# Optimization experiments

Measured on AMD Instinct MI355X. Metric: run time of the kernel, lower is better.

## Reference

```python
import jax, jax.numpy as jnp
import numpy as np

B, T, V, S = 64, 512, 1296, 32
BLANK = 0
NEG = jnp.float32(-1e30)  # log-space -inf surrogate (keeps grads finite)


def setup_inputs() -> dict:
    key = jax.random.key(0)
    k1, k2 = jax.random.split(key)
    logits = jax.random.normal(k1, (B, T, V), dtype=jnp.float32)
    # CTC targets must not contain the blank index (0)
    targets = jax.random.randint(k2, (B, S), 1, V).astype(jnp.int64)
    input_lengths = jnp.full((B,), T, dtype=jnp.int32)
    target_lengths = jnp.full((B,), S, dtype=jnp.int32)
    return {"logits": logits, "targets": targets,
            "input_lengths": input_lengths, "target_lengths": target_lengths}


def _ctc_loss(log_probs, targets, input_lengths, target_lengths):
    """CTC negative log-likelihood, reduction='mean' (per-sample / target_len, then batch mean)."""
    Bb, Tt, Vv = log_probs.shape
    Ss = targets.shape[1]
    L = 2 * Ss + 1  # extended label sequence: blank-interleaved

    ext = jnp.full((Bb, L), BLANK, dtype=targets.dtype).at[:, 1::2].set(targets)  # (B,L)
    # log-prob of each extended label at each time: (B,T,L)
    lp_ext = jnp.take_along_axis(log_probs, jnp.broadcast_to(ext[:, None, :], (Bb, Tt, L)), axis=2)

    # transition s-2 -> s allowed iff ext[s] is non-blank (s odd) and ext[s] != ext[s-2]
    pos = jnp.arange(L)
    ext_m2 = jnp.pad(ext, ((0, 0), (2, 0)), constant_values=-1)[:, :L]
    skip_ok = (pos[None, :] % 2 == 1) & (ext != ext_m2)  # (B,L)

    alpha0 = (jnp.full((Bb, L), NEG)
              .at[:, 0].set(lp_ext[:, 0, 0])
              .at[:, 1].set(lp_ext[:, 0, 1]))

    def step(alpha, lp_t):
        a1 = alpha
        a2 = jnp.pad(alpha[:, :-1], ((0, 0), (1, 0)), constant_values=NEG)
        a3 = jnp.where(skip_ok, jnp.pad(alpha[:, :-2], ((0, 0), (2, 0)), constant_values=NEG), NEG)
        new = jnp.logaddexp(jnp.logaddexp(a1, a2), a3) + lp_t
        return new, new

    _, alphas_rest = jax.lax.scan(step, alpha0, jnp.swapaxes(lp_ext, 0, 1)[1:])  # (T-1,B,L)
    alphas = jnp.concatenate([alpha0[None], alphas_rest], axis=0)  # (T,B,L)

    bi = jnp.arange(Bb)
    alpha_last = alphas[input_lengths - 1, bi]  # (B,L)
    l_end = alpha_last[bi, 2 * target_lengths]       # final blank
    l_lab = alpha_last[bi, 2 * target_lengths - 1]   # final label
    nll = -jnp.logaddexp(l_end, l_lab)               # (B,)
    nll = jnp.where(jnp.isinf(nll) | (nll > 1e29), 0.0, nll)  # zero_infinity=True
    return jnp.mean(nll / target_lengths.astype(nll.dtype))    # reduction='mean'


def reference(logits, targets, input_lengths, target_lengths):
    log_probs = jax.nn.log_softmax(logits, axis=-1)
    return _ctc_loss(log_probs, targets, input_lengths, target_lengths)
```

## Files before the change

### kernel.cpp

```cpp
#include <hip/hip_runtime.h>
#include <math.h>

#define BB 64
#define TT 512
#define VV 1296
#define SS 32
#define LL 65
#define LP 72
#define NEGV (-1e30f)
#define LOG2E 1.44269504088896340736f
#define LN2   0.69314718055994530942f

#define EXP2(x) __builtin_amdgcn_exp2f(x)
#define LOG2(x) __builtin_amdgcn_logf(x)

__global__ __launch_bounds__(256) void k_lse_gather(
    const float* __restrict__ logits,
    const int* __restrict__ targets,
    float* __restrict__ lp_ext)
{
    const int wid  = threadIdx.x >> 6;
    const int lane = threadIdx.x & 63;
    const int bt   = blockIdx.x * 4 + wid;
    const int b    = bt >> 9;

    const float* row = logits + (size_t)bt * VV;
    const float4* row4 = (const float4*)row;

    float4 v[5];
    #pragma unroll
    for (int k = 0; k < 5; ++k) v[k] = row4[lane + 64 * k];
    float4 vx = row4[320 + (lane & 3)];
    if (lane >= 4) { vx.x = NEGV; vx.y = NEGV; vx.z = NEGV; vx.w = NEGV; }

    float m = fmaxf(fmaxf(v[0].x, v[0].y), fmaxf(v[0].z, v[0].w));
    #pragma unroll
    for (int k = 1; k < 5; ++k)
        m = fmaxf(m, fmaxf(fmaxf(v[k].x, v[k].y), fmaxf(v[k].z, v[k].w)));
    m = fmaxf(m, fmaxf(fmaxf(vx.x, vx.y), fmaxf(vx.z, vx.w)));
    #pragma unroll
    for (int off = 1; off < 64; off <<= 1) m = fmaxf(m, __shfl_xor(m, off, 64));

    float s = 0.f;
    #pragma unroll
    for (int k = 0; k < 5; ++k)
        s += __expf(v[k].x - m) + __expf(v[k].y - m) +
             __expf(v[k].z - m) + __expf(v[k].w - m);
    s += __expf(vx.x - m) + __expf(vx.y - m) +
         __expf(vx.z - m) + __expf(vx.w - m);
    #pragma unroll
    for (int off = 1; off < 64; off <<= 1) s += __shfl_xor(s, off, 64);

    const float norm = m + __logf(s);

    const int lab = (lane & 1) ? targets[b * SS + (lane >> 1)] : 0;
    const float lp2 = (row[lab] - norm) * LOG2E;
    float* dst = lp_ext + (size_t)bt * LP;
    dst[lane] = lp2;
    if (lane == 0) dst[64] = lp2;
}

#define PF 12

__global__ __launch_bounds__(64) void k_alpha(
    const float* __restrict__ lp_ext,
    const int* __restrict__ targets,
    const int* __restrict__ in_len,
    const int* __restrict__ tgt_len,
    float* __restrict__ partial)
{
    const int b    = blockIdx.x;
    const int lane = threadIdx.x;
    const float* lp = lp_ext + (size_t)b * TT * LP;
    const int Ti = in_len[b];
    const int Sb = tgt_len[b];

    bool skip = false;
    if ((lane & 1) && lane >= 3) {
        const int j = lane >> 1;
        skip = (targets[b * SS + j] != targets[b * SS + j - 1]);
    }

    float alpha   = (lane == 0) ? lp[0] : (lane == 1 ? lp[1] : NEGV);
    float alpha64 = NEGV;

    float buf[PF];
    #pragma unroll
    for (int i = 0; i < PF; ++i) {
        int tt = 1 + i; if (tt > TT - 1) tt = TT - 1;
        buf[i] = lp[(size_t)tt * LP + lane];
    }

    int t = 1;

#define STEP(LPS)                                                            \
    {                                                                        \
        const float lps_  = (LPS);                                           \
        const float lpbk_ = __shfl(lps_, 0, 64);               \
        const float a1_ = alpha;                                             \
        float a2_ = __shfl_up(alpha, 1, 64);                                 \
        float a3_ = __shfl_up(alpha, 2, 64);                                 \
        const float a63_ = __shfl(alpha, 63, 64);                            \
        if (lane == 0) a2_ = NEGV;                                           \
        if (lane < 2 || !skip) a3_ = NEGV;                                   \
        const float mx_ = fmaxf(a1_, fmaxf(a2_, a3_));                       \
        const float an_ = mx_ + LOG2(EXP2(a1_ - mx_) + EXP2(a2_ - mx_) +     \
                                     EXP2(a3_ - mx_)) + lps_;                \
        const float m2_ = fmaxf(alpha64, a63_);                              \
        alpha64 = m2_ + LOG2(EXP2(alpha64 - m2_) + EXP2(a63_ - m2_)) + lpbk_;\
        alpha = an_;                                                         \
    }

    while (t + PF <= Ti) {
        #pragma unroll
        for (int i = 0; i < PF; ++i) {
            const float cur = buf[i];
            int tp = t + i + PF; if (tp > TT - 1) tp = TT - 1;
            buf[i] = lp[(size_t)tp * LP + lane];
            STEP(cur);
        }
        t += PF;
    }
    #pragma unroll
    for (int i = 0; i < PF; ++i) {
        if (t < Ti) { STEP(buf[i]); ++t; }
    }
#undef STEP

    const float vll = __shfl(alpha, 2 * Sb - 1, 64);
    const float vle = (2 * Sb >= 64) ? alpha64 : __shfl(alpha, 2 * Sb, 64);

    if (lane == 0) {
        const float mx = fmaxf(vle, vll);
        float nll = -LN2 * (mx + LOG2(EXP2(vle - mx) + EXP2(vll - mx)));
        if (isinf(nll) || nll > 1e29f) nll = 0.f;
        partial[b] = nll / (float)Sb;
    }
}

__global__ __launch_bounds__(64) void k_mean(
    const float* __restrict__ partial, float* __restrict__ out)
{
    const int lane = threadIdx.x;
    float v = (lane < BB) ? partial[lane] : 0.f;
    #pragma unroll
    for (int off = 32; off; off >>= 1) v += __shfl_down(v, off, 64);
    if (lane == 0) out[0] = v / (float)BB;
}

extern "C" void kernel_launch(void* const* d_in, const int* in_sizes, int n_in,
                              void* d_out, int out_size, void* d_ws, size_t ws_size,
                              hipStream_t stream) {
    const float* logits   = (const float*)d_in[0];
    const int*   targets  = (const int*)d_in[1];
    const int*   in_len   = (const int*)d_in[2];
    const int*   tgt_len  = (const int*)d_in[3];
    float*       out      = (float*)d_out;

    float* lp_ext  = (float*)d_ws;
    float* partial = lp_ext + (size_t)BB * TT * LP;

    k_lse_gather<<<BB * TT / 4, 256, 0, stream>>>(logits, targets, lp_ext);
    k_alpha<<<BB, 64, 0, stream>>>(lp_ext, targets, in_len, tgt_len, partial);
    k_mean<<<1, 64, 0, stream>>>(partial, out);
}
```

Baseline: 293.2 us.

## Interleave lp_ext in time groups of four, use readlane, fold mean via atomics

```diff
diff --git a/kernel.cpp b/kernel.cpp
--- a/kernel.cpp
+++ b/kernel.cpp
@@ -5,8 +5,8 @@
 #define TT 512
 #define VV 1296
 #define SS 32
-#define LL 65
-#define LP 72
+#define NST 64
+#define NG  (TT/4)
 #define NEGV (-1e30f)
 #define LOG2E 1.44269504088896340736f
 #define LN2   0.69314718055994530942f
@@ -14,15 +14,26 @@
 #define EXP2(x) __builtin_amdgcn_exp2f(x)
 #define LOG2(x) __builtin_amdgcn_logf(x)
 
+__device__ __forceinline__ float readlane_f(float v, int l) {
+    return __int_as_float(__builtin_amdgcn_readlane(__float_as_int(v), l));
+}
+__device__ __forceinline__ float readlane0_f(float v) {
+    return __int_as_float(__builtin_amdgcn_readfirstlane(__float_as_int(v)));
+}
+
 __global__ __launch_bounds__(256) void k_lse_gather(
     const float* __restrict__ logits,
     const int* __restrict__ targets,
-    float* __restrict__ lp_ext)
+    float* __restrict__ lp_ext,
+    float* __restrict__ out)
 {
     const int wid  = threadIdx.x >> 6;
     const int lane = threadIdx.x & 63;
     const int bt   = blockIdx.x * 4 + wid;
     const int b    = bt >> 9;
+    const int t    = bt & (TT - 1);
+
+    if (bt == 0 && lane == 0) out[0] = 0.f;
 
     const float* row = logits + (size_t)bt * VV;
     const float4* row4 = (const float4*)row;
@@ -55,23 +66,21 @@
 
     const int lab = (lane & 1) ? targets[b * SS + (lane >> 1)] : 0;
     const float lp2 = (row[lab] - norm) * LOG2E;
-    float* dst = lp_ext + (size_t)bt * LP;
-    dst[lane] = lp2;
-    if (lane == 0) dst[64] = lp2;
+    lp_ext[(((size_t)b * NG + (t >> 2)) * NST + lane) * 4 + (t & 3)] = lp2;
 }
 
-#define PF 12
+#define PFV 6
 
 __global__ __launch_bounds__(64) void k_alpha(
     const float* __restrict__ lp_ext,
     const int* __restrict__ targets,
     const int* __restrict__ in_len,
     const int* __restrict__ tgt_len,
-    float* __restrict__ partial)
+    float* __restrict__ out)
 {
     const int b    = blockIdx.x;
     const int lane = threadIdx.x;
-    const float* lp = lp_ext + (size_t)b * TT * LP;
+    const float4* lpv = (const float4*)(lp_ext + (size_t)b * NG * NST * 4);
     const int Ti = in_len[b];
     const int Sb = tgt_len[b];
 
@@ -81,28 +90,21 @@
         skip = (targets[b * SS + j] != targets[b * SS + j - 1]);
     }
 
-    float alpha   = (lane == 0) ? lp[0] : (lane == 1 ? lp[1] : NEGV);
+    float4 g0 = lpv[lane];
+
+    float alpha   = (lane < 2) ? g0.x : NEGV;
     float alpha64 = NEGV;
-
-    float buf[PF];
-    #pragma unroll
-    for (int i = 0; i < PF; ++i) {
-        int tt = 1 + i; if (tt > TT - 1) tt = TT - 1;
-        buf[i] = lp[(size_t)tt * LP + lane];
-    }
-
-    int t = 1;
 
 #define STEP(LPS)                                                            \
     {                                                                        \
         const float lps_  = (LPS);                                           \
-        const float lpbk_ = __shfl(lps_, 0, 64);               \
+        const float lpbk_ = readlane0_f(lps_);                 \
         const float a1_ = alpha;                                             \
         float a2_ = __shfl_up(alpha, 1, 64);                                 \
         float a3_ = __shfl_up(alpha, 2, 64);                                 \
-        const float a63_ = __shfl(alpha, 63, 64);                            \
+        const float a63_ = readlane_f(alpha, 63);                            \
         if (lane == 0) a2_ = NEGV;                                           \
-        if (lane < 2 || !skip) a3_ = NEGV;                                   \
+        if (!skip) a3_ = NEGV;                                               \
         const float mx_ = fmaxf(a1_, fmaxf(a2_, a3_));                       \
         const float an_ = mx_ + LOG2(EXP2(a1_ - mx_) + EXP2(a2_ - mx_) +     \
                                      EXP2(a3_ - mx_)) + lps_;                \
@@ -111,19 +113,40 @@
         alpha = an_;                                                         \
     }
 
-    while (t + PF <= Ti) {
+    if (1 < Ti) STEP(g0.y);
+    if (2 < Ti) STEP(g0.z);
+    if (3 < Ti) STEP(g0.w);
+
+    float4 bufv[PFV];
+    #pragma unroll
+    for (int i = 0; i < PFV; ++i)
+        bufv[i] = lpv[(1 + i) * NST + lane];
+
+    int g = 1;
+    while (g + PFV <= NG) {
         #pragma unroll
-        for (int i = 0; i < PF; ++i) {
-            const float cur = buf[i];
-            int tp = t + i + PF; if (tp > TT - 1) tp = TT - 1;
-            buf[i] = lp[(size_t)tp * LP + lane];
-            STEP(cur);
+        for (int i = 0; i < PFV; ++i) {
+            const float4 cur = bufv[i];
+            int gp = g + i + PFV; if (gp > NG - 1) gp = NG - 1;
+            bufv[i] = lpv[(size_t)gp * NST + lane];
+            const int t0 = (g + i) * 4;
+            if (t0 + 0 < Ti) STEP(cur.x);
+            if (t0 + 1 < Ti) STEP(cur.y);
+            if (t0 + 2 < Ti) STEP(cur.z);
+            if (t0 + 3 < Ti) STEP(cur.w);
         }
-        t += PF;
+        g += PFV;
     }
     #pragma unroll
-    for (int i = 0; i < PF; ++i) {
-        if (t < Ti) { STEP(buf[i]); ++t; }
+    for (int i = 0; i < PFV; ++i) {
+        if (g + i <= NG - 1) {
+            const float4 cur = bufv[i];
+            const int t0 = (g + i) * 4;
+            if (t0 + 0 < Ti) STEP(cur.x);
+            if (t0 + 1 < Ti) STEP(cur.y);
+            if (t0 + 2 < Ti) STEP(cur.z);
+            if (t0 + 3 < Ti) STEP(cur.w);
+        }
     }
 #undef STEP
 
@@ -134,18 +157,8 @@
         const float mx = fmaxf(vle, vll);
         float nll = -LN2 * (mx + LOG2(EXP2(vle - mx) + EXP2(vll - mx)));
         if (isinf(nll) || nll > 1e29f) nll = 0.f;
-        partial[b] = nll / (float)Sb;
+        atomicAdd(out, nll / ((float)Sb * (float)BB));
     }
-}
-
-__global__ __launch_bounds__(64) void k_mean(
-    const float* __restrict__ partial, float* __restrict__ out)
-{
-    const int lane = threadIdx.x;
-    float v = (lane < BB) ? partial[lane] : 0.f;
-    #pragma unroll
-    for (int off = 32; off; off >>= 1) v += __shfl_down(v, off, 64);
-    if (lane == 0) out[0] = v / (float)BB;
 }
 
 extern "C" void kernel_launch(void* const* d_in, const int* in_sizes, int n_in,
@@ -157,10 +170,8 @@
     const int*   tgt_len  = (const int*)d_in[3];
     float*       out      = (float*)d_out;
 
-    float* lp_ext  = (float*)d_ws;
-    float* partial = lp_ext + (size_t)BB * TT * LP;
+    float* lp_ext = (float*)d_ws;
 
-    k_lse_gather<<<BB * TT / 4, 256, 0, stream>>>(logits, targets, lp_ext);
-    k_alpha<<<BB, 64, 0, stream>>>(lp_ext, targets, in_len, tgt_len, partial);
-    k_mean<<<1, 64, 0, stream>>>(partial, out);
+    k_lse_gather<<<BB * TT / 4, 256, 0, stream>>>(logits, targets, lp_ext, out);
+    k_alpha<<<BB, 64, 0, stream>>>(lp_ext, targets, in_len, tgt_len, out);
 }
```

After: 303.6 us. 1.04x slower.
